# Kernel tuning notes

Measured on AMD Instinct MI355X. Metric: run time of the kernel, lower is better.

## Reference

```python
import jax, jax.numpy as jnp
import numpy as np

INPUT_DIM = 1024
EMBED_DIMS = 128


def setup_inputs() -> dict:
    key = jax.random.key(0)
    ks = jax.random.split(key, 7)
    s_in = 1.0 / np.sqrt(INPUT_DIM)
    x = jax.random.normal(ks[0], (4, 4096, INPUT_DIM), dtype=jnp.float32)
    Wq = jax.random.uniform(ks[1], (INPUT_DIM, EMBED_DIMS), jnp.float32, -s_in, s_in)
    bq = jax.random.uniform(ks[2], (EMBED_DIMS,), jnp.float32, -s_in, s_in)
    Wk = jax.random.uniform(ks[3], (INPUT_DIM, EMBED_DIMS), jnp.float32, -s_in, s_in)
    bk = jax.random.uniform(ks[4], (EMBED_DIMS,), jnp.float32, -s_in, s_in)
    Wv = jax.random.uniform(ks[5], (INPUT_DIM, EMBED_DIMS), jnp.float32, -s_in, s_in)
    bv = jax.random.uniform(ks[6], (EMBED_DIMS,), jnp.float32, -s_in, s_in)
    return {"x": x, "Wq": Wq, "bq": bq, "Wk": Wk, "bk": bk, "Wv": Wv, "bv": bv}


def reference(x, Wq, bq, Wk, bk, Wv, bv):
    # x: [B, L, C]
    Q = jnp.einsum('blc,cd->bld', x, Wq) + bq  # [B, L, D]
    K = jnp.einsum('blc,cd->bld', x, Wk) + bk
    V = jnp.einsum('blc,cd->bld', x, Wv) + bv
    d_k = Q.shape[-1]
    scores = jnp.einsum('bld,bmd->blm', Q, K) / jnp.sqrt(jnp.float32(d_k))  # [B, L, L]
    attn = jax.nn.softmax(scores, axis=-1)
    return jnp.einsum('blm,bmd->bld', attn, V)  # [B, L, D]
```

## Files before the change

### kernel.cpp

```cpp
#include <hip/hip_runtime.h>
#include <stdint.h>

typedef __bf16 bf16;
typedef __bf16 bf16x8 __attribute__((ext_vector_type(8)));
typedef __bf16 bf16x4 __attribute__((ext_vector_type(4)));
typedef _Float16 f16;
typedef f16 f16x8 __attribute__((ext_vector_type(8)));
typedef f16 f16x4 __attribute__((ext_vector_type(4)));
typedef float f32x4 __attribute__((ext_vector_type(4)));
typedef float f32x16 __attribute__((ext_vector_type(16)));
typedef uint32_t u32x4 __attribute__((ext_vector_type(4)));

#define LQ    16384
#define CDIM  1024
#define DDIM  128
#define NSPLIT 4
#define QS 0.12751741f

static __device__ __forceinline__ uint32_t pkrtz(float a, float b) {
  return __builtin_bit_cast(uint32_t, __builtin_amdgcn_cvt_pkrtz(a, b));
}

static __device__ __forceinline__ void lds_barrier() {
  asm volatile("s_waitcnt lgkmcnt(0)" ::: "memory");
  __builtin_amdgcn_s_barrier();
}

__global__ void prep_kernel(const float* __restrict__ Wq, const float* __restrict__ Wk,
                            const float* __restrict__ Wv, const float* __restrict__ bq,
                            const float* __restrict__ bk, const float* __restrict__ bv,
                            bf16* __restrict__ Wt, float* __restrict__ bias_all) {
  int idx = blockIdx.x * 256 + threadIdx.x;
  int p = idx >> 17;
  int rem = idx & 131071;
  int k = rem >> 7, n = rem & 127;
  const float* W = (p == 0) ? Wq : (p == 1) ? Wk : Wv;
  float s = (p == 0) ? QS : 1.0f;
  Wt[(size_t)(p * 128 + n) * CDIM + k] = (bf16)(W[rem] * s);
  if (idx < 384) {
    int pp = idx >> 7, nn = idx & 127;
    const float* b = (pp == 0) ? bq : (pp == 1) ? bk : bv;
    bias_all[idx] = b[nn] * ((pp == 0) ? QS : 1.0f);
  }
}

__global__ __launch_bounds__(512, 1) void qkv_gemm(
    const float* __restrict__ x, const bf16* __restrict__ Wt,
    const float* __restrict__ bias_all,
    bf16* __restrict__ Qw, bf16* __restrict__ Kw, f16* __restrict__ Vtw) {
  __shared__ bf16 As[2][64 * 64];
  __shared__ bf16 Bs[2][384 * 64];
  const int t = threadIdx.x;
  const int w = t >> 6;
  const int lane = t & 63;
  const int l31 = lane & 31;
  const int hi = lane >> 5;
  const int m0 = blockIdx.x * 64;
  const int m_off = (w & 1) * 32;
  const int n_off = ((w >> 1) & 3) * 32;

  const f32x16 z16 = {0.f,0.f,0.f,0.f,0.f,0.f,0.f,0.f,0.f,0.f,0.f,0.f,0.f,0.f,0.f,0.f};
  f32x16 acc[3];
  acc[0] = z16; acc[1] = z16; acc[2] = z16;

  const int srow = t >> 3;
  const int g = t & 7;
  const int sgoff = (g ^ (srow & 7)) * 8;
  const int scol = g * 8;

  float4 xa[2];
  bf16x8 wa[6];
  {
    const float* p = &x[(size_t)(m0 + srow) * CDIM + scol];
    xa[0] = *(const float4*)p;
    xa[1] = *(const float4*)(p + 4);
  }
#pragma unroll
  for (int c = 0; c < 6; c++)
    wa[c] = *(const bf16x8*)&Wt[(size_t)(c * 64 + srow) * CDIM + scol];

  for (int kc = 0; kc < 16; kc++) {
    bf16* Ab = As[kc & 1];
    bf16* Bb = Bs[kc & 1];
    {
      bf16x8 v;
      v[0] = (bf16)xa[0].x; v[1] = (bf16)xa[0].y;
      v[2] = (bf16)xa[0].z; v[3] = (bf16)xa[0].w;
      v[4] = (bf16)xa[1].x; v[5] = (bf16)xa[1].y;
      v[6] = (bf16)xa[1].z; v[7] = (bf16)xa[1].w;
      *(bf16x8*)&Ab[srow * 64 + sgoff] = v;
    }
#pragma unroll
    for (int c = 0; c < 6; c++)
      *(bf16x8*)&Bb[(c * 64 + srow) * 64 + sgoff] = wa[c];

    const int kn = (kc < 15 ? kc + 1 : 15) * 64;
    {
      const float* p = &x[(size_t)(m0 + srow) * CDIM + kn + scol];
      xa[0] = *(const float4*)p;
      xa[1] = *(const float4*)(p + 4);
    }
#pragma unroll
    for (int c = 0; c < 6; c++)
      wa[c] = *(const bf16x8*)&Wt[(size_t)(c * 64 + srow) * CDIM + kn + scol];

    lds_barrier();

#pragma unroll
    for (int ks = 0; ks < 4; ks++) {
      const int rg = ((ks * 2 + hi) ^ (l31 & 7)) * 8;
      bf16x8 af = *(const bf16x8*)&Ab[(m_off + l31) * 64 + rg];
#pragma unroll
      for (int p = 0; p < 3; p++) {
        bf16x8 bfr = *(const bf16x8*)&Bb[(p * 128 + n_off + l31) * 64 + rg];
        acc[p] = __builtin_amdgcn_mfma_f32_32x32x16_bf16(af, bfr, acc[p], 0, 0, 0);
      }
    }
    __builtin_amdgcn_s_barrier();
  }

  const int n = n_off + l31;
#pragma unroll
  for (int p = 0; p < 3; p++) {
    const float bias = bias_all[p * 128 + n];
    if (p < 2) {
      bf16* outp = (p == 0) ? Qw : Kw;
#pragma unroll
      for (int r = 0; r < 16; r++) {
        int m = m0 + m_off + (r & 3) + 8 * (r >> 2) + 4 * hi;
        outp[(size_t)m * DDIM + n] = (bf16)(acc[p][r] + bias);
      }
    } else {
#pragma unroll
      for (int gq = 0; gq < 4; gq++) {
        int mbase = m0 + m_off + 8 * gq + 4 * hi;
        f16x4 pv;
#pragma unroll
        for (int r = 0; r < 4; r++) pv[r] = (f16)(acc[p][gq * 4 + r] + bias);
        *(f16x4*)&Vtw[(size_t)n * LQ + mbase] = pv;
      }
    }
  }
}

__global__ __launch_bounds__(256, 2) void flash_kernel(
    const bf16* __restrict__ Qw, const bf16* __restrict__ Kw, const f16* __restrict__ Vtw,
    bf16* __restrict__ Opb, float* __restrict__ lp) {
  __shared__ bf16 Kl[2][64 * 136];
  __shared__ f16  Vl[2][128 * 72];

  const int t = threadIdx.x;
  const int w = t >> 6;
  const int lane = t & 63;
  const int l31 = lane & 31;
  const int hi = lane >> 5;
  const int lin = blockIdx.y * 128 + blockIdx.x;
  const int logical = ((lin & 7) << 6) + (lin >> 3);
  const int qb = logical & 127;
  const int sp = logical >> 7;
  const int batch = qb >> 5;
  const int q0w = qb * 128 + w * 32;
  const int kv_base = batch * 4096 + sp * 1024;

  bf16x8 qf[8];
#pragma unroll
  for (int ks = 0; ks < 8; ks++)
    qf[ks] = *(const bf16x8*)&Qw[(size_t)(q0w + l31) * DDIM + ks * 16 + hi * 8];

  const f32x16 z16 = {0.f,0.f,0.f,0.f,0.f,0.f,0.f,0.f,0.f,0.f,0.f,0.f,0.f,0.f,0.f,0.f};
  f32x16 o[4];
  o[0] = z16; o[1] = z16; o[2] = z16; o[3] = z16;
  f32x16 liacc = z16;

  f16x8 ones;
#pragma unroll
  for (int i = 0; i < 8; i++) ones[i] = (f16)1.f;

  const int kr = t >> 4;
  const int kcol = (t & 15) << 3;
  const int vr = t >> 3;
  const int vcol = (t & 7) << 3;

  bf16x8 ka[4];
  f16x8 va[4];
  f16x8 pa[4];

#pragma unroll
  for (int c = 0; c < 4; c++)
    ka[c] = *(const bf16x8*)&Kw[(size_t)(kv_base + c * 16 + kr) * DDIM + kcol];
#pragma unroll
  for (int c = 0; c < 4; c++)
    va[c] = *(const f16x8*)&Vtw[(size_t)(c * 32 + vr) * LQ + kv_base + vcol];

#pragma unroll
  for (int c = 0; c < 4; c++)
    *(bf16x8*)&Kl[0][(c * 16 + kr) * 136 + kcol] = ka[c];
#pragma unroll
  for (int c = 0; c < 4; c++)
    *(f16x8*)&Vl[0][(c * 32 + vr) * 72 + vcol] = va[c];

#pragma unroll
  for (int c = 0; c < 4; c++)
    ka[c] = *(const bf16x8*)&Kw[(size_t)(kv_base + 64 + c * 16 + kr) * DDIM + kcol];
#pragma unroll
  for (int c = 0; c < 4; c++)
    va[c] = *(const f16x8*)&Vtw[(size_t)(c * 32 + vr) * LQ + kv_base + 64 + vcol];

  lds_barrier();

  f32x16 sv0 = z16, sv1 = z16;
  __builtin_amdgcn_s_setprio(1);
#pragma unroll
  for (int ks = 0; ks < 8; ks++) {
    bf16x8 kf0 = *(const bf16x8*)&Kl[0][l31 * 136 + ks * 16 + hi * 8];
    bf16x8 kf1 = *(const bf16x8*)&Kl[0][(32 + l31) * 136 + ks * 16 + hi * 8];
    sv0 = __builtin_amdgcn_mfma_f32_32x32x16_bf16(kf0, qf[ks], sv0, 0, 0, 0);
    sv1 = __builtin_amdgcn_mfma_f32_32x32x16_bf16(kf1, qf[ks], sv1, 0, 0, 0);
  }
  __builtin_amdgcn_s_setprio(0);
#pragma unroll
  for (int r = 0; r < 16; r++) {
    sv0[r] = __builtin_amdgcn_exp2f(sv0[r]);
    sv1[r] = __builtin_amdgcn_exp2f(sv1[r]);
  }
#pragma unroll
  for (int sl = 0; sl < 4; sl++) {
    const int b = (sl & 1) * 8;
    float s0 = (sl >> 1) ? sv1[b + 0] : sv0[b + 0];
    float s1 = (sl >> 1) ? sv1[b + 1] : sv0[b + 1];
    float s2 = (sl >> 1) ? sv1[b + 2] : sv0[b + 2];
    float s3 = (sl >> 1) ? sv1[b + 3] : sv0[b + 3];
    float s4 = (sl >> 1) ? sv1[b + 4] : sv0[b + 4];
    float s5 = (sl >> 1) ? sv1[b + 5] : sv0[b + 5];
    float s6 = (sl >> 1) ? sv1[b + 6] : sv0[b + 6];
    float s7 = (sl >> 1) ? sv1[b + 7] : sv0[b + 7];
    uint32_t a0 = pkrtz(s0, s1);
    uint32_t a1 = pkrtz(s2, s3);
    uint32_t a2 = pkrtz(s4, s5);
    uint32_t a3 = pkrtz(s6, s7);
    asm("v_permlane32_swap_b32 %0, %1" : "+v"(a0), "+v"(a2));
    asm("v_permlane32_swap_b32 %0, %1" : "+v"(a1), "+v"(a3));
    u32x4 aw; aw.x = a0; aw.y = a1; aw.z = a2; aw.w = a3;
    pa[sl] = __builtin_bit_cast(f16x8, aw);
  }

  for (int tile = 0; tile < 15; tile++) {
    bf16* Kb = Kl[(tile + 1) & 1];
    f16*  Vb = Vl[(tile + 1) & 1];
    f16*  Vp = Vl[tile & 1];
#pragma unroll
    for (int c = 0; c < 4; c++)
      *(bf16x8*)&Kb[(c * 16 + kr) * 136 + kcol] = ka[c];
#pragma unroll
    for (int c = 0; c < 4; c++)
      *(f16x8*)&Vb[(c * 32 + vr) * 72 + vcol] = va[c];

    const int kvn = kv_base + (tile < 14 ? tile + 2 : 15) * 64;
#pragma unroll
    for (int c = 0; c < 4; c++)
      ka[c] = *(const bf16x8*)&Kw[(size_t)(kvn + c * 16 + kr) * DDIM + kcol];
#pragma unroll
    for (int c = 0; c < 4; c++)
      va[c] = *(const f16x8*)&Vtw[(size_t)(c * 32 + vr) * LQ + kvn + vcol];

    lds_barrier();

    sv0 = z16; sv1 = z16;
    __builtin_amdgcn_s_setprio(1);
#pragma unroll
    for (int i = 0; i < 4; i++) {
      bf16x8 kf0a = *(const bf16x8*)&Kb[l31 * 136 + (2 * i) * 16 + hi * 8];
      bf16x8 kf1a = *(const bf16x8*)&Kb[(32 + l31) * 136 + (2 * i) * 16 + hi * 8];
      bf16x8 kf0b = *(const bf16x8*)&Kb[l31 * 136 + (2 * i + 1) * 16 + hi * 8];
      bf16x8 kf1b = *(const bf16x8*)&Kb[(32 + l31) * 136 + (2 * i + 1) * 16 + hi * 8];
      sv0 = __builtin_amdgcn_mfma_f32_32x32x16_bf16(kf0a, qf[2 * i], sv0, 0, 0, 0);
      sv1 = __builtin_amdgcn_mfma_f32_32x32x16_bf16(kf1a, qf[2 * i], sv1, 0, 0, 0);
      const int koff = (i >> 1) * 32 + (i & 1) * 16 + hi * 8;
#pragma unroll
      for (int dt = 0; dt < 4; dt++) {
        f16x8 vf = *(const f16x8*)&Vp[(dt * 32 + l31) * 72 + koff];
        o[dt] = __builtin_amdgcn_mfma_f32_32x32x16_f16(pa[i], vf, o[dt], 0, 0, 0);
      }
      liacc = __builtin_amdgcn_mfma_f32_32x32x16_f16(pa[i], ones, liacc, 0, 0, 0);
      sv0 = __builtin_amdgcn_mfma_f32_32x32x16_bf16(kf0b, qf[2 * i + 1], sv0, 0, 0, 0);
      sv1 = __builtin_amdgcn_mfma_f32_32x32x16_bf16(kf1b, qf[2 * i + 1], sv1, 0, 0, 0);
    }
    __builtin_amdgcn_s_setprio(0);

#pragma unroll
    for (int r = 0; r < 16; r++) {
      sv0[r] = __builtin_amdgcn_exp2f(sv0[r]);
      sv1[r] = __builtin_amdgcn_exp2f(sv1[r]);
    }
#pragma unroll
    for (int sl = 0; sl < 4; sl++) {
      const int b = (sl & 1) * 8;
      float s0 = (sl >> 1) ? sv1[b + 0] : sv0[b + 0];
      float s1 = (sl >> 1) ? sv1[b + 1] : sv0[b + 1];
      float s2 = (sl >> 1) ? sv1[b + 2] : sv0[b + 2];
      float s3 = (sl >> 1) ? sv1[b + 3] : sv0[b + 3];
      float s4 = (sl >> 1) ? sv1[b + 4] : sv0[b + 4];
      float s5 = (sl >> 1) ? sv1[b + 5] : sv0[b + 5];
      float s6 = (sl >> 1) ? sv1[b + 6] : sv0[b + 6];
      float s7 = (sl >> 1) ? sv1[b + 7] : sv0[b + 7];
      uint32_t a0 = pkrtz(s0, s1);
      uint32_t a1 = pkrtz(s2, s3);
      uint32_t a2 = pkrtz(s4, s5);
      uint32_t a3 = pkrtz(s6, s7);
      asm("v_permlane32_swap_b32 %0, %1" : "+v"(a0), "+v"(a2));
      asm("v_permlane32_swap_b32 %0, %1" : "+v"(a1), "+v"(a3));
      u32x4 aw; aw.x = a0; aw.y = a1; aw.z = a2; aw.w = a3;
      pa[sl] = __builtin_bit_cast(f16x8, aw);
    }

    __builtin_amdgcn_s_barrier();
  }

  {
    f16* Vp = Vl[15 & 1];
    __builtin_amdgcn_s_setprio(1);
#pragma unroll
    for (int i = 0; i < 4; i++) {
      const int koff = (i >> 1) * 32 + (i & 1) * 16 + hi * 8;
#pragma unroll
      for (int dt = 0; dt < 4; dt++) {
        f16x8 vf = *(const f16x8*)&Vp[(dt * 32 + l31) * 72 + koff];
        o[dt] = __builtin_amdgcn_mfma_f32_32x32x16_f16(pa[i], vf, o[dt], 0, 0, 0);
      }
      liacc = __builtin_amdgcn_mfma_f32_32x32x16_f16(pa[i], ones, liacc, 0, 0, 0);
    }
    __builtin_amdgcn_s_setprio(0);
  }

  const size_t po = (size_t)sp * LQ * DDIM;
#pragma unroll
  for (int dt = 0; dt < 4; dt++)
#pragma unroll
    for (int r = 0; r < 16; r++) {
      int q = q0w + (r & 3) + 8 * (r >> 2) + 4 * hi;
      Opb[po + (size_t)q * DDIM + dt * 32 + l31] = (bf16)o[dt][r];
    }
  if (l31 == 0) {
#pragma unroll
    for (int r = 0; r < 16; r++)
      lp[(size_t)sp * LQ + q0w + (r & 3) + 8 * (r >> 2) + 4 * hi] = liacc[r];
  }
}

__global__ void combine_kernel(const bf16* __restrict__ Opb, const float* __restrict__ lp,
                               float* __restrict__ out) {
  int idx = blockIdx.x * 256 + threadIdx.x;
  int q = idx >> 5;
  int d = (idx & 31) * 4;
  float lsum = 0.f;
  float acc[4] = {0.f, 0.f, 0.f, 0.f};
#pragma unroll
  for (int sp = 0; sp < NSPLIT; sp++) {
    lsum += lp[(size_t)sp * LQ + q];
    bf16x4 ov = *(const bf16x4*)&Opb[(size_t)sp * LQ * DDIM + (size_t)q * DDIM + d];
#pragma unroll
    for (int j = 0; j < 4; j++) acc[j] += (float)ov[j];
  }
  float inv = 1.0f / lsum;
  float4 r;
  r.x = acc[0] * inv; r.y = acc[1] * inv; r.z = acc[2] * inv; r.w = acc[3] * inv;
  *(float4*)&out[(size_t)q * DDIM + d] = r;
}

extern "C" void kernel_launch(void* const* d_in, const int* in_sizes, int n_in,
                              void* d_out, int out_size, void* d_ws, size_t ws_size,
                              hipStream_t stream) {
  const float* x  = (const float*)d_in[0];
  const float* Wq = (const float*)d_in[1];
  const float* bq = (const float*)d_in[2];
  const float* Wk = (const float*)d_in[3];
  const float* bk = (const float*)d_in[4];
  const float* Wv = (const float*)d_in[5];
  const float* bv = (const float*)d_in[6];
  char* ws = (char*)d_ws;
  bf16* Qw   = (bf16*)(ws);
  bf16* Kw   = (bf16*)(ws + ((size_t)4 << 20));
  f16*  Vtw  = (f16*)(ws + ((size_t)8 << 20));
  bf16* Wt   = (bf16*)(ws + ((size_t)12 << 20));
  float* bias_all = (float*)(ws + ((size_t)12 << 20) + 786432);
  bf16* Opb  = (bf16*)(ws + ((size_t)13 << 20));
  float* lpp = (float*)(ws + ((size_t)29 << 20));
  float* out = (float*)d_out;

  prep_kernel<<<1536, 256, 0, stream>>>(Wq, Wk, Wv, bq, bk, bv, Wt, bias_all);
  qkv_gemm<<<256, 512, 0, stream>>>(x, Wt, bias_all, Qw, Kw, Vtw);
  flash_kernel<<<dim3(128, NSPLIT), 256, 0, stream>>>(Qw, Kw, Vtw, Opb, lpp);
  combine_kernel<<<2048, 256, 0, stream>>>(Opb, lpp, out);
}
```

Before: 169.2 us.

## Fuse prep, QKV GEMM, flash attention and combine into one cooperative kernel

Replaces the four separate launches (weight prep, QKV projection GEMM, split-KV flash attention, split combine) with a single cooperative kernel of 256 blocks × 512 threads, separated by grid-wide syncs. Shared memory is one raw buffer reused by each stage. The flash stage is reshaped so each block handles 256 queries with 8 waves instead of 128 queries with 4 waves. The trailing barrier in the GEMM k-loop is dropped, relying on the double-buffer plus the wait-and-barrier at the top of each step. The goal is to remove inter-kernel launch gaps and tail effects, at the cost of grid.sync overhead and forcing every stage to run with one 512-thread block per CU.

```diff
diff --git a/kernel.cpp b/kernel.cpp
--- a/kernel.cpp
+++ b/kernel.cpp
@@ -1,5 +1,8 @@
 #include <hip/hip_runtime.h>
+#include <hip/hip_cooperative_groups.h>
 #include <stdint.h>
+
+namespace cg = cooperative_groups;
 
 typedef __bf16 bf16;
 typedef __bf16 bf16x8 __attribute__((ext_vector_type(8)));
@@ -7,14 +10,12 @@
 typedef _Float16 f16;
 typedef f16 f16x8 __attribute__((ext_vector_type(8)));
 typedef f16 f16x4 __attribute__((ext_vector_type(4)));
-typedef float f32x4 __attribute__((ext_vector_type(4)));
 typedef float f32x16 __attribute__((ext_vector_type(16)));
 typedef uint32_t u32x4 __attribute__((ext_vector_type(4)));
 
 #define LQ    16384
 #define CDIM  1024
 #define DDIM  128
-#define NSPLIT 4
 #define QS 0.12751741f
 
 static __device__ __forceinline__ uint32_t pkrtz(float a, float b) {
@@ -26,267 +27,198 @@
   __builtin_amdgcn_s_barrier();
 }
 
-__global__ void prep_kernel(const float* __restrict__ Wq, const float* __restrict__ Wk,
-                            const float* __restrict__ Wv, const float* __restrict__ bq,
-                            const float* __restrict__ bk, const float* __restrict__ bv,
-                            bf16* __restrict__ Wt, float* __restrict__ bias_all) {
-  int idx = blockIdx.x * 256 + threadIdx.x;
-  int p = idx >> 17;
-  int rem = idx & 131071;
-  int k = rem >> 7, n = rem & 127;
-  const float* W = (p == 0) ? Wq : (p == 1) ? Wk : Wv;
-  float s = (p == 0) ? QS : 1.0f;
-  Wt[(size_t)(p * 128 + n) * CDIM + k] = (bf16)(W[rem] * s);
-  if (idx < 384) {
-    int pp = idx >> 7, nn = idx & 127;
-    const float* b = (pp == 0) ? bq : (pp == 1) ? bk : bv;
-    bias_all[idx] = b[nn] * ((pp == 0) ? QS : 1.0f);
-  }
-}
-
-__global__ __launch_bounds__(512, 1) void qkv_gemm(
-    const float* __restrict__ x, const bf16* __restrict__ Wt,
-    const float* __restrict__ bias_all,
-    bf16* __restrict__ Qw, bf16* __restrict__ Kw, f16* __restrict__ Vtw) {
-  __shared__ bf16 As[2][64 * 64];
-  __shared__ bf16 Bs[2][384 * 64];
+__global__ __launch_bounds__(512, 1) void fused_kernel(
+    const float* __restrict__ x,
+    const float* __restrict__ Wq, const float* __restrict__ bq,
+    const float* __restrict__ Wk, const float* __restrict__ bk,
+    const float* __restrict__ Wv, const float* __restrict__ bv,
+    bf16* __restrict__ Wt, float* __restrict__ bias_all,
+    bf16* __restrict__ Qw, bf16* __restrict__ Kw, f16* __restrict__ Vtw,
+    bf16* __restrict__ Opb, float* __restrict__ lp, float* __restrict__ out) {
+  __shared__ __align__(16) char smem[114688];
+  cg::grid_group grid = cg::this_grid();
+  const int b = blockIdx.x;
   const int t = threadIdx.x;
-  const int w = t >> 6;
   const int lane = t & 63;
   const int l31 = lane & 31;
   const int hi = lane >> 5;
-  const int m0 = blockIdx.x * 64;
-  const int m_off = (w & 1) * 32;
-  const int n_off = ((w >> 1) & 3) * 32;
+  const int w = t >> 6;
 
   const f32x16 z16 = {0.f,0.f,0.f,0.f,0.f,0.f,0.f,0.f,0.f,0.f,0.f,0.f,0.f,0.f,0.f,0.f};
-  f32x16 acc[3];
-  acc[0] = z16; acc[1] = z16; acc[2] = z16;
-
-  const int srow = t >> 3;
-  const int g = t & 7;
-  const int sgoff = (g ^ (srow & 7)) * 8;
-  const int scol = g * 8;
-
-  float4 xa[2];
-  bf16x8 wa[6];
+
   {
-    const float* p = &x[(size_t)(m0 + srow) * CDIM + scol];
-    xa[0] = *(const float4*)p;
-    xa[1] = *(const float4*)(p + 4);
+#pragma unroll
+    for (int i = 0; i < 3; i++) {
+      int idx = i * 131072 + b * 512 + t;
+      int p = idx >> 17;
+      int rem = idx & 131071;
+      int k = rem >> 7, n = rem & 127;
+      const float* W = (p == 0) ? Wq : (p == 1) ? Wk : Wv;
+      float s = (p == 0) ? QS : 1.0f;
+      Wt[(size_t)(p * 128 + n) * CDIM + k] = (bf16)(W[rem] * s);
+    }
+    int idx0 = b * 512 + t;
+    if (idx0 < 384) {
+      int pp = idx0 >> 7, nn = idx0 & 127;
+      const float* bb = (pp == 0) ? bq : (pp == 1) ? bk : bv;
+      bias_all[idx0] = bb[nn] * ((pp == 0) ? QS : 1.0f);
+    }
   }
-#pragma unroll
-  for (int c = 0; c < 6; c++)
-    wa[c] = *(const bf16x8*)&Wt[(size_t)(c * 64 + srow) * CDIM + scol];
-
-  for (int kc = 0; kc < 16; kc++) {
-    bf16* Ab = As[kc & 1];
-    bf16* Bb = Bs[kc & 1];
+  grid.sync();
+
+  {
+    bf16* As0 = (bf16*)smem;
+    bf16* Bs0 = (bf16*)(smem + 16384);
+    const int m0 = b * 64;
+    const int m_off = (w & 1) * 32;
+    const int n_off = ((w >> 1) & 3) * 32;
+
+    f32x16 acc[3];
+    acc[0] = z16; acc[1] = z16; acc[2] = z16;
+
+    const int srow = t >> 3;
+    const int g = t & 7;
+    const int sgoff = (g ^ (srow & 7)) * 8;
+    const int scol = g * 8;
+
+    float4 xa[2];
+    bf16x8 wa[6];
     {
-      bf16x8 v;
-      v[0] = (bf16)xa[0].x; v[1] = (bf16)xa[0].y;
-      v[2] = (bf16)xa[0].z; v[3] = (bf16)xa[0].w;
-      v[4] = (bf16)xa[1].x; v[5] = (bf16)xa[1].y;
-      v[6] = (bf16)xa[1].z; v[7] = (bf16)xa[1].w;
-      *(bf16x8*)&Ab[srow * 64 + sgoff] = v;
-    }
-#pragma unroll
-    for (int c = 0; c < 6; c++)
-      *(bf16x8*)&Bb[(c * 64 + srow) * 64 + sgoff] = wa[c];
-
-    const int kn = (kc < 15 ? kc + 1 : 15) * 64;
-    {
-      const float* p = &x[(size_t)(m0 + srow) * CDIM + kn + scol];
+      const float* p = &x[(size_t)(m0 + srow) * CDIM + scol];
       xa[0] = *(const float4*)p;
       xa[1] = *(const float4*)(p + 4);
     }
 #pragma unroll
     for (int c = 0; c < 6; c++)
-      wa[c] = *(const bf16x8*)&Wt[(size_t)(c * 64 + srow) * CDIM + kn + scol];
+      wa[c] = *(const bf16x8*)&Wt[(size_t)(c * 64 + srow) * CDIM + scol];
+
+    for (int kc = 0; kc < 16; kc++) {
+      bf16* Ab = As0 + (kc & 1) * 4096;
+      bf16* Bb = Bs0 + (kc & 1) * 24576;
+      {
+        bf16x8 v;
+        v[0] = (bf16)xa[0].x; v[1] = (bf16)xa[0].y;
+        v[2] = (bf16)xa[0].z; v[3] = (bf16)xa[0].w;
+        v[4] = (bf16)xa[1].x; v[5] = (bf16)xa[1].y;
+        v[6] = (bf16)xa[1].z; v[7] = (bf16)xa[1].w;
+        *(bf16x8*)&Ab[srow * 64 + sgoff] = v;
+      }
+#pragma unroll
+      for (int c = 0; c < 6; c++)
+        *(bf16x8*)&Bb[(c * 64 + srow) * 64 + sgoff] = wa[c];
+
+      const int kn = (kc < 15 ? kc + 1 : 15) * 64;
+      {
+        const float* p = &x[(size_t)(m0 + srow) * CDIM + kn + scol];
+        xa[0] = *(const float4*)p;
+        xa[1] = *(const float4*)(p + 4);
+      }
+#pragma unroll
+      for (int c = 0; c < 6; c++)
+        wa[c] = *(const bf16x8*)&Wt[(size_t)(c * 64 + srow) * CDIM + kn + scol];
+
+      lds_barrier();
+
+#pragma unroll
+      for (int ks = 0; ks < 4; ks++) {
+        const int rg = ((ks * 2 + hi) ^ (l31 & 7)) * 8;
+        bf16x8 af = *(const bf16x8*)&Ab[(m_off + l31) * 64 + rg];
+#pragma unroll
+        for (int p = 0; p < 3; p++) {
+          bf16x8 bfr = *(const bf16x8*)&Bb[(p * 128 + n_off + l31) * 64 + rg];
+          acc[p] = __builtin_amdgcn_mfma_f32_32x32x16_bf16(af, bfr, acc[p], 0, 0, 0);
+        }
+      }
+    }
+
+    const int n = n_off + l31;
+#pragma unroll
+    for (int p = 0; p < 3; p++) {
+      const float bias = bias_all[p * 128 + n];
+      if (p < 2) {
+        bf16* outp = (p == 0) ? Qw : Kw;
+#pragma unroll
+        for (int r = 0; r < 16; r++) {
+          int m = m0 + m_off + (r & 3) + 8 * (r >> 2) + 4 * hi;
+          outp[(size_t)m * DDIM + n] = (bf16)(acc[p][r] + bias);
+        }
+      } else {
+#pragma unroll
+        for (int gq = 0; gq < 4; gq++) {
+          int mbase = m0 + m_off + 8 * gq + 4 * hi;
+          f16x4 pv;
+#pragma unroll
+          for (int r = 0; r < 4; r++) pv[r] = (f16)(acc[p][gq * 4 + r] + bias);
+          *(f16x4*)&Vtw[(size_t)n * LQ + mbase] = pv;
+        }
+      }
+    }
+  }
+  grid.sync();
+
+  {
+    bf16* Kl0 = (bf16*)smem;
+    f16*  Vl0 = (f16*)(smem + 34816);
+    const int logical = ((b & 7) << 5) + (b >> 3);
+    const int qbp = logical & 63;
+    const int sp = logical >> 6;
+    const int batch = qbp >> 4;
+    const int q0w = qbp * 256 + w * 32;
+    const int kv_base = batch * 4096 + sp * 1024;
+
+    bf16x8 qf[8];
+#pragma unroll
+    for (int ks = 0; ks < 8; ks++)
+      qf[ks] = *(const bf16x8*)&Qw[(size_t)(q0w + l31) * DDIM + ks * 16 + hi * 8];
+
+    f32x16 o[4];
+    o[0] = z16; o[1] = z16; o[2] = z16; o[3] = z16;
+    f32x16 liacc = z16;
+
+    f16x8 ones;
+#pragma unroll
+    for (int i = 0; i < 8; i++) ones[i] = (f16)1.f;
+
+    const int kr = t >> 4;
+    const int kc2 = (t & 15) << 3;
+    const int vr = t >> 3;
+    const int vc2 = (t & 7) << 3;
+
+    bf16x8 ka[2];
+    f16x8 va[2];
+    f16x8 pa[4];
+
+#pragma unroll
+    for (int c = 0; c < 2; c++)
+      ka[c] = *(const bf16x8*)&Kw[(size_t)(kv_base + c * 32 + kr) * DDIM + kc2];
+#pragma unroll
+    for (int c = 0; c < 2; c++)
+      va[c] = *(const f16x8*)&Vtw[(size_t)(c * 64 + vr) * LQ + kv_base + vc2];
+#pragma unroll
+    for (int c = 0; c < 2; c++)
+      *(bf16x8*)&Kl0[(c * 32 + kr) * 136 + kc2] = ka[c];
+#pragma unroll
+    for (int c = 0; c < 2; c++)
+      *(f16x8*)&Vl0[(c * 64 + vr) * 72 + vc2] = va[c];
+#pragma unroll
+    for (int c = 0; c < 2; c++)
+      ka[c] = *(const bf16x8*)&Kw[(size_t)(kv_base + 64 + c * 32 + kr) * DDIM + kc2];
+#pragma unroll
+    for (int c = 0; c < 2; c++)
+      va[c] = *(const f16x8*)&Vtw[(size_t)(c * 64 + vr) * LQ + kv_base + 64 + vc2];
 
     lds_barrier();
 
-#pragma unroll
-    for (int ks = 0; ks < 4; ks++) {
-      const int rg = ((ks * 2 + hi) ^ (l31 & 7)) * 8;
-      bf16x8 af = *(const bf16x8*)&Ab[(m_off + l31) * 64 + rg];
-#pragma unroll
-      for (int p = 0; p < 3; p++) {
-        bf16x8 bfr = *(const bf16x8*)&Bb[(p * 128 + n_off + l31) * 64 + rg];
-        acc[p] = __builtin_amdgcn_mfma_f32_32x32x16_bf16(af, bfr, acc[p], 0, 0, 0);
-      }
-    }
-    __builtin_amdgcn_s_barrier();
-  }
-
-  const int n = n_off + l31;
-#pragma unroll
-  for (int p = 0; p < 3; p++) {
-    const float bias = bias_all[p * 128 + n];
-    if (p < 2) {
-      bf16* outp = (p == 0) ? Qw : Kw;
-#pragma unroll
-      for (int r = 0; r < 16; r++) {
-        int m = m0 + m_off + (r & 3) + 8 * (r >> 2) + 4 * hi;
-        outp[(size_t)m * DDIM + n] = (bf16)(acc[p][r] + bias);
-      }
-    } else {
-#pragma unroll
-      for (int gq = 0; gq < 4; gq++) {
-        int mbase = m0 + m_off + 8 * gq + 4 * hi;
-        f16x4 pv;
-#pragma unroll
-        for (int r = 0; r < 4; r++) pv[r] = (f16)(acc[p][gq * 4 + r] + bias);
-        *(f16x4*)&Vtw[(size_t)n * LQ + mbase] = pv;
-      }
-    }
-  }
-}
-
-__global__ __launch_bounds__(256, 2) void flash_kernel(
-    const bf16* __restrict__ Qw, const bf16* __restrict__ Kw, const f16* __restrict__ Vtw,
-    bf16* __restrict__ Opb, float* __restrict__ lp) {
-  __shared__ bf16 Kl[2][64 * 136];
-  __shared__ f16  Vl[2][128 * 72];
-
-  const int t = threadIdx.x;
-  const int w = t >> 6;
-  const int lane = t & 63;
-  const int l31 = lane & 31;
-  const int hi = lane >> 5;
-  const int lin = blockIdx.y * 128 + blockIdx.x;
-  const int logical = ((lin & 7) << 6) + (lin >> 3);
-  const int qb = logical & 127;
-  const int sp = logical >> 7;
-  const int batch = qb >> 5;
-  const int q0w = qb * 128 + w * 32;
-  const int kv_base = batch * 4096 + sp * 1024;
-
-  bf16x8 qf[8];
-#pragma unroll
-  for (int ks = 0; ks < 8; ks++)
-    qf[ks] = *(const bf16x8*)&Qw[(size_t)(q0w + l31) * DDIM + ks * 16 + hi * 8];
-
-  const f32x16 z16 = {0.f,0.f,0.f,0.f,0.f,0.f,0.f,0.f,0.f,0.f,0.f,0.f,0.f,0.f,0.f,0.f};
-  f32x16 o[4];
-  o[0] = z16; o[1] = z16; o[2] = z16; o[3] = z16;
-  f32x16 liacc = z16;
-
-  f16x8 ones;
-#pragma unroll
-  for (int i = 0; i < 8; i++) ones[i] = (f16)1.f;
-
-  const int kr = t >> 4;
-  const int kcol = (t & 15) << 3;
-  const int vr = t >> 3;
-  const int vcol = (t & 7) << 3;
-
-  bf16x8 ka[4];
-  f16x8 va[4];
-  f16x8 pa[4];
-
-#pragma unroll
-  for (int c = 0; c < 4; c++)
-    ka[c] = *(const bf16x8*)&Kw[(size_t)(kv_base + c * 16 + kr) * DDIM + kcol];
-#pragma unroll
-  for (int c = 0; c < 4; c++)
-    va[c] = *(const f16x8*)&Vtw[(size_t)(c * 32 + vr) * LQ + kv_base + vcol];
-
-#pragma unroll
-  for (int c = 0; c < 4; c++)
-    *(bf16x8*)&Kl[0][(c * 16 + kr) * 136 + kcol] = ka[c];
-#pragma unroll
-  for (int c = 0; c < 4; c++)
-    *(f16x8*)&Vl[0][(c * 32 + vr) * 72 + vcol] = va[c];
-
-#pragma unroll
-  for (int c = 0; c < 4; c++)
-    ka[c] = *(const bf16x8*)&Kw[(size_t)(kv_base + 64 + c * 16 + kr) * DDIM + kcol];
-#pragma unroll
-  for (int c = 0; c < 4; c++)
-    va[c] = *(const f16x8*)&Vtw[(size_t)(c * 32 + vr) * LQ + kv_base + 64 + vcol];
-
-  lds_barrier();
-
-  f32x16 sv0 = z16, sv1 = z16;
-  __builtin_amdgcn_s_setprio(1);
-#pragma unroll
-  for (int ks = 0; ks < 8; ks++) {
-    bf16x8 kf0 = *(const bf16x8*)&Kl[0][l31 * 136 + ks * 16 + hi * 8];
-    bf16x8 kf1 = *(const bf16x8*)&Kl[0][(32 + l31) * 136 + ks * 16 + hi * 8];
-    sv0 = __builtin_amdgcn_mfma_f32_32x32x16_bf16(kf0, qf[ks], sv0, 0, 0, 0);
-    sv1 = __builtin_amdgcn_mfma_f32_32x32x16_bf16(kf1, qf[ks], sv1, 0, 0, 0);
-  }
-  __builtin_amdgcn_s_setprio(0);
-#pragma unroll
-  for (int r = 0; r < 16; r++) {
-    sv0[r] = __builtin_amdgcn_exp2f(sv0[r]);
-    sv1[r] = __builtin_amdgcn_exp2f(sv1[r]);
-  }
-#pragma unroll
-  for (int sl = 0; sl < 4; sl++) {
-    const int b = (sl & 1) * 8;
-    float s0 = (sl >> 1) ? sv1[b + 0] : sv0[b + 0];
-    float s1 = (sl >> 1) ? sv1[b + 1] : sv0[b + 1];
-    float s2 = (sl >> 1) ? sv1[b + 2] : sv0[b + 2];
-    float s3 = (sl >> 1) ? sv1[b + 3] : sv0[b + 3];
-    float s4 = (sl >> 1) ? sv1[b + 4] : sv0[b + 4];
-    float s5 = (sl >> 1) ? sv1[b + 5] : sv0[b + 5];
-    float s6 = (sl >> 1) ? sv1[b + 6] : sv0[b + 6];
-    float s7 = (sl >> 1) ? sv1[b + 7] : sv0[b + 7];
-    uint32_t a0 = pkrtz(s0, s1);
-    uint32_t a1 = pkrtz(s2, s3);
-    uint32_t a2 = pkrtz(s4, s5);
-    uint32_t a3 = pkrtz(s6, s7);
-    asm("v_permlane32_swap_b32 %0, %1" : "+v"(a0), "+v"(a2));
-    asm("v_permlane32_swap_b32 %0, %1" : "+v"(a1), "+v"(a3));
-    u32x4 aw; aw.x = a0; aw.y = a1; aw.z = a2; aw.w = a3;
-    pa[sl] = __builtin_bit_cast(f16x8, aw);
-  }
-
-  for (int tile = 0; tile < 15; tile++) {
-    bf16* Kb = Kl[(tile + 1) & 1];
-    f16*  Vb = Vl[(tile + 1) & 1];
-    f16*  Vp = Vl[tile & 1];
-#pragma unroll
-    for (int c = 0; c < 4; c++)
-      *(bf16x8*)&Kb[(c * 16 + kr) * 136 + kcol] = ka[c];
-#pragma unroll
-    for (int c = 0; c < 4; c++)
-      *(f16x8*)&Vb[(c * 32 + vr) * 72 + vcol] = va[c];
-
-    const int kvn = kv_base + (tile < 14 ? tile + 2 : 15) * 64;
-#pragma unroll
-    for (int c = 0; c < 4; c++)
-      ka[c] = *(const bf16x8*)&Kw[(size_t)(kvn + c * 16 + kr) * DDIM + kcol];
-#pragma unroll
-    for (int c = 0; c < 4; c++)
-      va[c] = *(const f16x8*)&Vtw[(size_t)(c * 32 + vr) * LQ + kvn + vcol];
-
-    lds_barrier();
-
-    sv0 = z16; sv1 = z16;
+    f32x16 sv0 = z16, sv1 = z16;
     __builtin_amdgcn_s_setprio(1);
 #pragma unroll
-    for (int i = 0; i < 4; i++) {
-      bf16x8 kf0a = *(const bf16x8*)&Kb[l31 * 136 + (2 * i) * 16 + hi * 8];
-      bf16x8 kf1a = *(const bf16x8*)&Kb[(32 + l31) * 136 + (2 * i) * 16 + hi * 8];
-      bf16x8 kf0b = *(const bf16x8*)&Kb[l31 * 136 + (2 * i + 1) * 16 + hi * 8];
-      bf16x8 kf1b = *(const bf16x8*)&Kb[(32 + l31) * 136 + (2 * i + 1) * 16 + hi * 8];
-      sv0 = __builtin_amdgcn_mfma_f32_32x32x16_bf16(kf0a, qf[2 * i], sv0, 0, 0, 0);
-      sv1 = __builtin_amdgcn_mfma_f32_32x32x16_bf16(kf1a, qf[2 * i], sv1, 0, 0, 0);
-      const int koff = (i >> 1) * 32 + (i & 1) * 16 + hi * 8;
-#pragma unroll
-      for (int dt = 0; dt < 4; dt++) {
-        f16x8 vf = *(const f16x8*)&Vp[(dt * 32 + l31) * 72 + koff];
-        o[dt] = __builtin_amdgcn_mfma_f32_32x32x16_f16(pa[i], vf, o[dt], 0, 0, 0);
-      }
-      liacc = __builtin_amdgcn_mfma_f32_32x32x16_f16(pa[i], ones, liacc, 0, 0, 0);
-      sv0 = __builtin_amdgcn_mfma_f32_32x32x16_bf16(kf0b, qf[2 * i + 1], sv0, 0, 0, 0);
-      sv1 = __builtin_amdgcn_mfma_f32_32x32x16_bf16(kf1b, qf[2 * i + 1], sv1, 0, 0, 0);
+    for (int ks = 0; ks < 8; ks++) {
+      bf16x8 kf0 = *(const bf16x8*)&Kl0[l31 * 136 + ks * 16 + hi * 8];
+      bf16x8 kf1 = *(const bf16x8*)&Kl0[(32 + l31) * 136 + ks * 16 + hi * 8];
+      sv0 = __builtin_amdgcn_mfma_f32_32x32x16_bf16(kf0, qf[ks], sv0, 0, 0, 0);
+      sv1 = __builtin_amdgcn_mfma_f32_32x32x16_bf16(kf1, qf[ks], sv1, 0, 0, 0);
     }
     __builtin_amdgcn_s_setprio(0);
-
 #pragma unroll
     for (int r = 0; r < 16; r++) {
       sv0[r] = __builtin_amdgcn_exp2f(sv0[r]);
@@ -294,15 +226,15 @@
     }
 #pragma unroll
     for (int sl = 0; sl < 4; sl++) {
-      const int b = (sl & 1) * 8;
-      float s0 = (sl >> 1) ? sv1[b + 0] : sv0[b + 0];
-      float s1 = (sl >> 1) ? sv1[b + 1] : sv0[b + 1];
-      float s2 = (sl >> 1) ? sv1[b + 2] : sv0[b + 2];
-      float s3 = (sl >> 1) ? sv1[b + 3] : sv0[b + 3];
-      float s4 = (sl >> 1) ? sv1[b + 4] : sv0[b + 4];
-      float s5 = (sl >> 1) ? sv1[b + 5] : sv0[b + 5];
-      float s6 = (sl >> 1) ? sv1[b + 6] : sv0[b + 6];
-      float s7 = (sl >> 1) ? sv1[b + 7] : sv0[b + 7];
+      const int bb = (sl & 1) * 8;
+      float s0 = (sl >> 1) ? sv1[bb + 0] : sv0[bb + 0];
+      float s1 = (sl >> 1) ? sv1[bb + 1] : sv0[bb + 1];
+      float s2 = (sl >> 1) ? sv1[bb + 2] : sv0[bb + 2];
+      float s3 = (sl >> 1) ? sv1[bb + 3] : sv0[bb + 3];
+      float s4 = (sl >> 1) ? sv1[bb + 4] : sv0[bb + 4];
+      float s5 = (sl >> 1) ? sv1[bb + 5] : sv0[bb + 5];
+      float s6 = (sl >> 1) ? sv1[bb + 6] : sv0[bb + 6];
+      float s7 = (sl >> 1) ? sv1[bb + 7] : sv0[bb + 7];
       uint32_t a0 = pkrtz(s0, s1);
       uint32_t a1 = pkrtz(s2, s3);
       uint32_t a2 = pkrtz(s4, s5);
@@ -313,58 +245,131 @@
       pa[sl] = __builtin_bit_cast(f16x8, aw);
     }
 
-    __builtin_amdgcn_s_barrier();
+    for (int tile = 0; tile < 15; tile++) {
+      bf16* Kb = Kl0 + ((tile + 1) & 1) * 8704;
+      f16*  Vb = Vl0 + ((tile + 1) & 1) * 9216;
+      f16*  Vp = Vl0 + (tile & 1) * 9216;
+#pragma unroll
+      for (int c = 0; c < 2; c++)
+        *(bf16x8*)&Kb[(c * 32 + kr) * 136 + kc2] = ka[c];
+#pragma unroll
+      for (int c = 0; c < 2; c++)
+        *(f16x8*)&Vb[(c * 64 + vr) * 72 + vc2] = va[c];
+
+      const int kvn = kv_base + (tile < 14 ? tile + 2 : 15) * 64;
+#pragma unroll
+      for (int c = 0; c < 2; c++)
+        ka[c] = *(const bf16x8*)&Kw[(size_t)(kvn + c * 32 + kr) * DDIM + kc2];
+#pragma unroll
+      for (int c = 0; c < 2; c++)
+        va[c] = *(const f16x8*)&Vtw[(size_t)(c * 64 + vr) * LQ + kvn + vc2];
+
+      lds_barrier();
+
+      sv0 = z16; sv1 = z16;
+      __builtin_amdgcn_s_setprio(1);
+#pragma unroll
+      for (int i = 0; i < 4; i++) {
+        bf16x8 kf0a = *(const bf16x8*)&Kb[l31 * 136 + (2 * i) * 16 + hi * 8];
+        bf16x8 kf1a = *(const bf16x8*)&Kb[(32 + l31) * 136 + (2 * i) * 16 + hi * 8];
+        bf16x8 kf0b = *(const bf16x8*)&Kb[l31 * 136 + (2 * i + 1) * 16 + hi * 8];
+        bf16x8 kf1b = *(const bf16x8*)&Kb[(32 + l31) * 136 + (2 * i + 1) * 16 + hi * 8];
+        sv0 = __builtin_amdgcn_mfma_f32_32x32x16_bf16(kf0a, qf[2 * i], sv0, 0, 0, 0);
+        sv1 = __builtin_amdgcn_mfma_f32_32x32x16_bf16(kf1a, qf[2 * i], sv1, 0, 0, 0);
+        const int koff = (i >> 1) * 32 + (i & 1) * 16 + hi * 8;
+#pragma unroll
+        for (int dt = 0; dt < 4; dt++) {
+          f16x8 vf = *(const f16x8*)&Vp[(dt * 32 + l31) * 72 + koff];
+          o[dt] = __builtin_amdgcn_mfma_f32_32x32x16_f16(pa[i], vf, o[dt], 0, 0, 0);
+        }
+        liacc = __builtin_amdgcn_mfma_f32_32x32x16_f16(pa[i], ones, liacc, 0, 0, 0);
+        sv0 = __builtin_amdgcn_mfma_f32_32x32x16_bf16(kf0b, qf[2 * i + 1], sv0, 0, 0, 0);
+        sv1 = __builtin_amdgcn_mfma_f32_32x32x16_bf16(kf1b, qf[2 * i + 1], sv1, 0, 0, 0);
+      }
+      __builtin_amdgcn_s_setprio(0);
+
+#pragma unroll
+      for (int r = 0; r < 16; r++) {
+        sv0[r] = __builtin_amdgcn_exp2f(sv0[r]);
+        sv1[r] = __builtin_amdgcn_exp2f(sv1[r]);
+      }
+#pragma unroll
+      for (int sl = 0; sl < 4; sl++) {
+        const int bb = (sl & 1) * 8;
+        float s0 = (sl >> 1) ? sv1[bb + 0] : sv0[bb + 0];
+        float s1 = (sl >> 1) ? sv1[bb + 1] : sv0[bb + 1];
+        float s2 = (sl >> 1) ? sv1[bb + 2] : sv0[bb + 2];
+        float s3 = (sl >> 1) ? sv1[bb + 3] : sv0[bb + 3];
+        float s4 = (sl >> 1) ? sv1[bb + 4] : sv0[bb + 4];
+        float s5 = (sl >> 1) ? sv1[bb + 5] : sv0[bb + 5];
+        float s6 = (sl >> 1) ? sv1[bb + 6] : sv0[bb + 6];
+        float s7 = (sl >> 1) ? sv1[bb + 7] : sv0[bb + 7];
+        uint32_t a0 = pkrtz(s0, s1);
+        uint32_t a1 = pkrtz(s2, s3);
+        uint32_t a2 = pkrtz(s4, s5);
+        uint32_t a3 = pkrtz(s6, s7);
+        asm("v_permlane32_swap_b32 %0, %1" : "+v"(a0), "+v"(a2));
+        asm("v_permlane32_swap_b32 %0, %1" : "+v"(a1), "+v"(a3));
+        u32x4 aw; aw.x = a0; aw.y = a1; aw.z = a2; aw.w = a3;
+        pa[sl] = __builtin_bit_cast(f16x8, aw);
+      }
+
+      __builtin_amdgcn_s_barrier();
+    }
+
+    {
+      f16* Vp = Vl0 + 9216;
+      __builtin_amdgcn_s_setprio(1);
+#pragma unroll
+      for (int i = 0; i < 4; i++) {
+        const int koff = (i >> 1) * 32 + (i & 1) * 16 + hi * 8;
+#pragma unroll
+        for (int dt = 0; dt < 4; dt++) {
+          f16x8 vf = *(const f16x8*)&Vp[(dt * 32 + l31) * 72 + koff];
+          o[dt] = __builtin_amdgcn_mfma_f32_32x32x16_f16(pa[i], vf, o[dt], 0, 0, 0);
+        }
+        liacc = __builtin_amdgcn_mfma_f32_32x32x16_f16(pa[i], ones, liacc, 0, 0, 0);
+      }
+      __builtin_amdgcn_s_setprio(0);
+    }
+
+    const size_t po = (size_t)sp * LQ * DDIM;
+#pragma unroll
+    for (int dt = 0; dt < 4; dt++)
+#pragma unroll
+      for (int r = 0; r < 16; r++) {
+        int q = q0w + (r & 3) + 8 * (r >> 2) + 4 * hi;
+        Opb[po + (size_t)q * DDIM + dt * 32 + l31] = (bf16)o[dt][r];
+      }
+    if (l31 == 0) {
+#pragma unroll
+      for (int r = 0; r < 16; r++)
+        lp[(size_t)sp * LQ + q0w + (r & 3) + 8 * (r >> 2) + 4 * hi] = liacc[r];
+    }
   }
+  grid.sync();
 
   {
-    f16* Vp = Vl[15 & 1];
-    __builtin_amdgcn_s_setprio(1);
 #pragma unroll
     for (int i = 0; i < 4; i++) {
-      const int koff = (i >> 1) * 32 + (i & 1) * 16 + hi * 8;
-#pragma unroll
-      for (int dt = 0; dt < 4; dt++) {
-        f16x8 vf = *(const f16x8*)&Vp[(dt * 32 + l31) * 72 + koff];
-        o[dt] = __builtin_amdgcn_mfma_f32_32x32x16_f16(pa[i], vf, o[dt], 0, 0, 0);
-      }
-      liacc = __builtin_amdgcn_mfma_f32_32x32x16_f16(pa[i], ones, liacc, 0, 0, 0);
-    }
-    __builtin_amdgcn_s_setprio(0);
+      int idx = i * 131072 + b * 512 + t;
+      int q = idx >> 5;
+      int d = (idx & 31) * 4;
+      float lsum = 0.f;
+      float a4[4] = {0.f, 0.f, 0.f, 0.f};
+#pragma unroll
+      for (int sp2 = 0; sp2 < 4; sp2++) {
+        lsum += lp[(size_t)sp2 * LQ + q];
+        bf16x4 ov = *(const bf16x4*)&Opb[(size_t)sp2 * LQ * DDIM + (size_t)q * DDIM + d];
+#pragma unroll
+        for (int j = 0; j < 4; j++) a4[j] += (float)ov[j];
+      }
+      float inv = 1.0f / lsum;
+      float4 r;
+      r.x = a4[0] * inv; r.y = a4[1] * inv; r.z = a4[2] * inv; r.w = a4[3] * inv;
+      *(float4*)&out[(size_t)q * DDIM + d] = r;
+    }
   }
-
-  const size_t po = (size_t)sp * LQ * DDIM;
-#pragma unroll
-  for (int dt = 0; dt < 4; dt++)
-#pragma unroll
-    for (int r = 0; r < 16; r++) {
-      int q = q0w + (r & 3) + 8 * (r >> 2) + 4 * hi;
-      Opb[po + (size_t)q * DDIM + dt * 32 + l31] = (bf16)o[dt][r];
-    }
-  if (l31 == 0) {
-#pragma unroll
-    for (int r = 0; r < 16; r++)
-      lp[(size_t)sp * LQ + q0w + (r & 3) + 8 * (r >> 2) + 4 * hi] = liacc[r];
-  }
-}
-
-__global__ void combine_kernel(const bf16* __restrict__ Opb, const float* __restrict__ lp,
-                               float* __restrict__ out) {
-  int idx = blockIdx.x * 256 + threadIdx.x;
-  int q = idx >> 5;
-  int d = (idx & 31) * 4;
-  float lsum = 0.f;
-  float acc[4] = {0.f, 0.f, 0.f, 0.f};
-#pragma unroll
-  for (int sp = 0; sp < NSPLIT; sp++) {
-    lsum += lp[(size_t)sp * LQ + q];
-    bf16x4 ov = *(const bf16x4*)&Opb[(size_t)sp * LQ * DDIM + (size_t)q * DDIM + d];
-#pragma unroll
-    for (int j = 0; j < 4; j++) acc[j] += (float)ov[j];
-  }
-  float inv = 1.0f / lsum;
-  float4 r;
-  r.x = acc[0] * inv; r.y = acc[1] * inv; r.z = acc[2] * inv; r.w = acc[3] * inv;
-  *(float4*)&out[(size_t)q * DDIM + d] = r;
 }
 
 extern "C" void kernel_launch(void* const* d_in, const int* in_sizes, int n_in,
@@ -387,8 +392,10 @@
   float* lpp = (float*)(ws + ((size_t)29 << 20));
   float* out = (float*)d_out;
 
-  prep_kernel<<<1536, 256, 0, stream>>>(Wq, Wk, Wv, bq, bk, bv, Wt, bias_all);
-  qkv_gemm<<<256, 512, 0, stream>>>(x, Wt, bias_all, Qw, Kw, Vtw);
-  flash_kernel<<<dim3(128, NSPLIT), 256, 0, stream>>>(Qw, Kw, Vtw, Opb, lpp);
-  combine_kernel<<<2048, 256, 0, stream>>>(Opb, lpp, out);
+  void* args[] = {(void*)&x,  (void*)&Wq, (void*)&bq, (void*)&Wk, (void*)&bk,
+                  (void*)&Wv, (void*)&bv, (void*)&Wt, (void*)&bias_all,
+                  (void*)&Qw, (void*)&Kw, (void*)&Vtw, (void*)&Opb, (void*)&lpp,
+                  (void*)&out};
+  hipLaunchCooperativeKernel((const void*)fused_kernel, dim3(256), dim3(512),
+                             args, 0, stream);
 }
```

Result: slower. 279.5 us (+65.3%).

## Load weight tiles directly into LDS and restructure QKV projection double-buffering

Applied to the files above, without the earlier changes.

Weight tiles for the QKV projection GEMM now go straight from global memory into LDS with global_load_lds instead of passing through registers. The main loop is reordered so the next tile's loads are issued before the MFMA work on the current tile. The converted x tile is written to the alternate buffer afterwards, leaving one barrier per iteration. This frees registers and overlaps loads with compute, but it depends on the LDS-direct writes landing correctly with the XOR swizzle and on the barrier and waitcnt handling of asynchronous LDS loads.

```diff
diff --git a/kernel.cpp b/kernel.cpp
--- a/kernel.cpp
+++ b/kernel.cpp
@@ -7,7 +7,6 @@
 typedef _Float16 f16;
 typedef f16 f16x8 __attribute__((ext_vector_type(8)));
 typedef f16 f16x4 __attribute__((ext_vector_type(4)));
-typedef float f32x4 __attribute__((ext_vector_type(4)));
 typedef float f32x16 __attribute__((ext_vector_type(16)));
 typedef uint32_t u32x4 __attribute__((ext_vector_type(4)));
 
@@ -24,6 +23,12 @@
 static __device__ __forceinline__ void lds_barrier() {
   asm volatile("s_waitcnt lgkmcnt(0)" ::: "memory");
   __builtin_amdgcn_s_barrier();
+}
+
+static __device__ __forceinline__ void gload_lds16(const void* g, void* l) {
+  __builtin_amdgcn_global_load_lds(
+      (__attribute__((address_space(1))) void*)g,
+      (__attribute__((address_space(3))) void*)l, 16, 0, 0);
 }
 
 __global__ void prep_kernel(const float* __restrict__ Wq, const float* __restrict__ Wk,
@@ -68,8 +73,11 @@
   const int sgoff = (g ^ (srow & 7)) * 8;
   const int scol = g * 8;
 
+  const int lrow = lane >> 3;
+  const int lgr = (lane & 7) ^ lrow;
+  const bf16* bsrc = Wt + (size_t)(w * 48 + lrow) * CDIM + lgr * 8;
+
   float4 xa[2];
-  bf16x8 wa[6];
   {
     const float* p = &x[(size_t)(m0 + srow) * CDIM + scol];
     xa[0] = *(const float4*)p;
@@ -77,46 +85,53 @@
   }
 #pragma unroll
   for (int c = 0; c < 6; c++)
-    wa[c] = *(const bf16x8*)&Wt[(size_t)(c * 64 + srow) * CDIM + scol];
+    gload_lds16(bsrc + (size_t)c * 8 * CDIM, &Bs[0][(w * 48 + c * 8) * 64]);
+  {
+    bf16x8 v;
+    v[0] = (bf16)xa[0].x; v[1] = (bf16)xa[0].y;
+    v[2] = (bf16)xa[0].z; v[3] = (bf16)xa[0].w;
+    v[4] = (bf16)xa[1].x; v[5] = (bf16)xa[1].y;
+    v[6] = (bf16)xa[1].z; v[7] = (bf16)xa[1].w;
+    *(bf16x8*)&As[0][srow * 64 + sgoff] = v;
+  }
+  lds_barrier();
 
   for (int kc = 0; kc < 16; kc++) {
     bf16* Ab = As[kc & 1];
     bf16* Bb = Bs[kc & 1];
-    {
+
+    if (kc < 15) {
+      const bf16* s = bsrc + (kc + 1) * 64;
+      bf16* Bn = Bs[(kc + 1) & 1];
+#pragma unroll
+      for (int c = 0; c < 6; c++)
+        gload_lds16(s + (size_t)c * 8 * CDIM, &Bn[(w * 48 + c * 8) * 64]);
+      const float* p = &x[(size_t)(m0 + srow) * CDIM + (kc + 1) * 64 + scol];
+      xa[0] = *(const float4*)p;
+      xa[1] = *(const float4*)(p + 4);
+    }
+
+#pragma unroll
+    for (int ks = 0; ks < 4; ks++) {
+      const int rg = ((ks * 2 + hi) ^ (l31 & 7)) * 8;
+      bf16x8 af = *(const bf16x8*)&Ab[(m_off + l31) * 64 + rg];
+#pragma unroll
+      for (int p = 0; p < 3; p++) {
+        bf16x8 bfr = *(const bf16x8*)&Bb[(p * 128 + n_off + l31) * 64 + rg];
+        acc[p] = __builtin_amdgcn_mfma_f32_32x32x16_bf16(af, bfr, acc[p], 0, 0, 0);
+      }
+    }
+
+    if (kc < 15) {
+      bf16* An = As[(kc + 1) & 1];
       bf16x8 v;
       v[0] = (bf16)xa[0].x; v[1] = (bf16)xa[0].y;
       v[2] = (bf16)xa[0].z; v[3] = (bf16)xa[0].w;
       v[4] = (bf16)xa[1].x; v[5] = (bf16)xa[1].y;
       v[6] = (bf16)xa[1].z; v[7] = (bf16)xa[1].w;
-      *(bf16x8*)&Ab[srow * 64 + sgoff] = v;
-    }
-#pragma unroll
-    for (int c = 0; c < 6; c++)
-      *(bf16x8*)&Bb[(c * 64 + srow) * 64 + sgoff] = wa[c];
-
-    const int kn = (kc < 15 ? kc + 1 : 15) * 64;
-    {
-      const float* p = &x[(size_t)(m0 + srow) * CDIM + kn + scol];
-      xa[0] = *(const float4*)p;
-      xa[1] = *(const float4*)(p + 4);
-    }
-#pragma unroll
-    for (int c = 0; c < 6; c++)
-      wa[c] = *(const bf16x8*)&Wt[(size_t)(c * 64 + srow) * CDIM + kn + scol];
-
-    lds_barrier();
-
-#pragma unroll
-    for (int ks = 0; ks < 4; ks++) {
-      const int rg = ((ks * 2 + hi) ^ (l31 & 7)) * 8;
-      bf16x8 af = *(const bf16x8*)&Ab[(m_off + l31) * 64 + rg];
-#pragma unroll
-      for (int p = 0; p < 3; p++) {
-        bf16x8 bfr = *(const bf16x8*)&Bb[(p * 128 + n_off + l31) * 64 + rg];
-        acc[p] = __builtin_amdgcn_mfma_f32_32x32x16_bf16(af, bfr, acc[p], 0, 0, 0);
-      }
-    }
-    __builtin_amdgcn_s_barrier();
+      *(bf16x8*)&An[srow * 64 + sgoff] = v;
+      lds_barrier();
+    }
   }
 
   const int n = n_off + l31;
```

Result: no change. 170.9 us (+1.0%).
